# Optimization experiments

Measured on AMD Instinct MI355X. Metric: run time of the kernel, lower is better.

## Reference

```python
import jax, jax.numpy as jnp
import numpy as np

B, T, D = 2, 2048, 1024
H = 16
HD = D // H

def setup_inputs() -> dict:
    key = jax.random.key(0)
    ks = jax.random.split(key, 5)
    s = 1.0 / np.sqrt(D)
    return {
        "x": jax.random.normal(ks[0], (B, T, D), dtype=jnp.float32),
        "Wq": jax.random.normal(ks[1], (D, D), dtype=jnp.float32) * s,
        "bq": jnp.zeros((D,), jnp.float32),
        "Wk": jax.random.normal(ks[2], (D, D), dtype=jnp.float32) * s,
        "bk": jnp.zeros((D,), jnp.float32),
        "Wv": jax.random.normal(ks[3], (D, D), dtype=jnp.float32) * s,
        "bv": jnp.zeros((D,), jnp.float32),
        "Wo": jax.random.normal(ks[4], (D, D), dtype=jnp.float32) * s,
        "bo": jnp.zeros((D,), jnp.float32),
    }

def reference(x, Wq, bq, Wk, bk, Wv, bv, Wo, bo):
    # projections: torch Linear computes x @ W.T + b
    def split_heads(t):  # [B,T,D] -> [B,H,T,HD]
        return t.reshape(B, T, H, HD).transpose(0, 2, 1, 3)
    q = split_heads(x @ Wq.T + bq)
    k = split_heads(x @ Wk.T + bk)
    v = split_heads(x @ Wv.T + bv)
    scale = 1.0 / jnp.sqrt(jnp.asarray(HD, x.dtype))
    scores = jnp.einsum("bhtd,bhsd->bhts", q, k) * scale  # [B,H,T,T]
    causal = jnp.tril(jnp.ones((T, T), bool))
    scores = jnp.where(causal, scores, -jnp.inf)
    attn = jax.nn.softmax(scores, axis=-1)
    out = jnp.einsum("bhts,bhsd->bhtd", attn, v)  # [B,H,T,HD]
    out = out.transpose(0, 2, 1, 3).reshape(B, T, D)
    return out @ Wo.T + bo
```

## Files before the change

### kernel.cpp

```cpp
#include <hip/hip_runtime.h>
#include <hip/hip_bf16.h>

#define B_NUM 2
#define T_LEN 2048
#define D_DIM 1024
#define H_NUM 16
#define HD_DIM 64

#define Q_PRESCALE 0.18033688011112042f

using bf16x8 = __attribute__((ext_vector_type(8))) short;
using f32x4  = __attribute__((ext_vector_type(4))) float;
using u16x4  = __attribute__((ext_vector_type(4))) unsigned short;

__device__ __forceinline__ unsigned short f2bf(float f) {
    union { __hip_bfloat16 b; unsigned short u; } v;
    v.b = __float2bfloat16(f);
    return v.u;
}

__device__ __forceinline__ unsigned pack2bf(float a, float b) {
    union { __hip_bfloat162 h; unsigned u; } v;
    v.h = __float22bfloat162_rn(float2{a, b});
    return v.u;
}

__device__ __forceinline__ void gload16(const unsigned short* g, unsigned short* l) {
    __builtin_amdgcn_global_load_lds(
        (const __attribute__((address_space(1))) void*)g,
        (__attribute__((address_space(3))) void*)l, 16, 0, 0);
}

__global__ __launch_bounds__(256) void cvt5(
    const float* __restrict__ s0, const float* __restrict__ s1, const float* __restrict__ s2,
    const float* __restrict__ s3, const float* __restrict__ s4,
    unsigned short* __restrict__ d0, unsigned short* __restrict__ d1, unsigned short* __restrict__ d2,
    unsigned short* __restrict__ d3, unsigned short* __restrict__ d4,
    int c0, int c1, int c2, int c3, int c4)
{
    const float* src; unsigned short* dst; int cnt;
    switch (blockIdx.z) {
        case 0: src = s0; dst = d0; cnt = c0; break;
        case 1: src = s1; dst = d1; cnt = c1; break;
        case 2: src = s2; dst = d2; cnt = c2; break;
        case 3: src = s3; dst = d3; cnt = c3; break;
        default: src = s4; dst = d4; cnt = c4; break;
    }
    const int stride = gridDim.x * 256 * 4;
    for (int i = (blockIdx.x * 256 + threadIdx.x) * 4; i < cnt; i += stride) {
        float4 v = *(const float4*)(src + i);
        u16x4 o = { f2bf(v.x), f2bf(v.y), f2bf(v.z), f2bf(v.w) };
        *(u16x4*)(dst + i) = o;
    }
}

__device__ __forceinline__ void tile128(
    const unsigned short* __restrict__ A, const unsigned short* __restrict__ Bm,
    int m0, int n0, int K, unsigned short* lds, f32x4 acc[4][4])
{
    const int tid  = threadIdx.x;
    const int lane = tid & 63, w = tid >> 6;
    const int g = lane >> 4, c = lane & 15;
    const int wr = w >> 1, wc = w & 1;
    const int srow = lane >> 2;
    const int sch  = lane & 3;
    const int scsw = sch ^ ((srow >> 1) & 3);
    const int chunk = w * 2;
    const int row0 = chunk * 16 + srow;
    const int row1 = row0 + 16;
    const int rsw = (c >> 1) & 3;

    #pragma unroll
    for (int mi = 0; mi < 4; ++mi)
        #pragma unroll
        for (int ni = 0; ni < 4; ++ni)
            acc[mi][ni] = (f32x4){0.f, 0.f, 0.f, 0.f};

    const unsigned short* gA0 = A  + (size_t)(m0 + row0) * K + scsw * 8;
    const unsigned short* gA1 = A  + (size_t)(m0 + row1) * K + scsw * 8;
    const unsigned short* gB0 = Bm + (size_t)(n0 + row0) * K + scsw * 8;
    const unsigned short* gB1 = Bm + (size_t)(n0 + row1) * K + scsw * 8;

    auto stage = [&](int buf, int k0) {
        unsigned short* bA = lds + buf * 8192;
        unsigned short* bB = bA + 4096;
        gload16(gA0 + k0, bA + chunk * 512);
        gload16(gA1 + k0, bA + (chunk + 1) * 512);
        gload16(gB0 + k0, bB + chunk * 512);
        gload16(gB1 + k0, bB + (chunk + 1) * 512);
    };

    auto kstep = [&](int buf) {
        __builtin_amdgcn_s_barrier();
        asm volatile("" ::: "memory");
        const unsigned short* bA = lds + buf * 8192;
        const unsigned short* bB = bA + 4096;
        bf16x8 af[4], bfr[4];
        #pragma unroll
        for (int mi = 0; mi < 4; ++mi)
            af[mi] = *(const bf16x8*)(bA + (wr * 64 + mi * 16 + c) * 32 + (g ^ rsw) * 8);
        #pragma unroll
        for (int ni = 0; ni < 4; ++ni)
            bfr[ni] = *(const bf16x8*)(bB + (wc * 64 + ni * 16 + c) * 32 + (g ^ rsw) * 8);
        #pragma unroll
        for (int mi = 0; mi < 4; ++mi)
            #pragma unroll
            for (int ni = 0; ni < 4; ++ni)
                acc[mi][ni] = __builtin_amdgcn_mfma_f32_16x16x32_bf16(af[mi], bfr[ni], acc[mi][ni], 0, 0, 0);
        asm volatile("s_waitcnt lgkmcnt(0)" ::: "memory");
        __builtin_amdgcn_s_barrier();
    };

    const int nsteps = K / 32;
    stage(0, 0);
    stage(1, 32);
    int buf = 0;
    #pragma unroll 1
    for (int t = 0; t + 2 < nsteps; ++t) {
        int nb = buf + 2; if (nb >= 3) nb -= 3;
        stage(nb, (t + 2) * 32);
        asm volatile("s_waitcnt vmcnt(8)" ::: "memory");
        kstep(buf);
        ++buf; if (buf == 3) buf = 0;
    }
    asm volatile("s_waitcnt vmcnt(4)" ::: "memory");
    kstep(buf);
    ++buf; if (buf == 3) buf = 0;
    asm volatile("s_waitcnt vmcnt(0)" ::: "memory");
    kstep(buf);
}

__global__ __launch_bounds__(256) void gemm_qkv(
    const unsigned short* __restrict__ X,
    const unsigned short* __restrict__ Wq, const unsigned short* __restrict__ Wk,
    const unsigned short* __restrict__ Wv,
    const float* __restrict__ bq, const float* __restrict__ bk, const float* __restrict__ bv,
    unsigned short* __restrict__ Oq, unsigned short* __restrict__ Ok, unsigned short* __restrict__ OvT)
{
    __shared__ __align__(16) unsigned short lds[3 * 8192];
    const int xcd = blockIdx.x & 7;
    const int s   = blockIdx.x >> 3;
    const int mt  = (xcd >> 1) * 8 + s / 12;
    const int rr  = (xcd & 1) * 12 + s % 12;
    const int z   = rr >> 3;
    const int nt  = rr & 7;

    const int lane = threadIdx.x & 63, w = threadIdx.x >> 6;
    const int g = lane >> 4, c = lane & 15;
    const int wr = w >> 1, wc = w & 1;
    f32x4 acc[4][4];

    if (z < 2) {
        const unsigned short* W = z ? Wk : Wq;
        const float* bias       = z ? bk : bq;
        unsigned short* Ob      = z ? Ok : Oq;
        const float oscale      = z ? 1.0f : Q_PRESCALE;
        const int m0 = mt * 128, n0 = nt * 128;
        tile128(X, W, m0, n0, D_DIM, lds, acc);
        #pragma unroll
        for (int mi = 0; mi < 4; ++mi) {
            #pragma unroll
            for (int ni = 0; ni < 4; ++ni) {
                const int col = n0 + wc * 64 + ni * 16 + c;
                const int h = col >> 6, hd = col & 63;
                const float bb = bias[col];
                #pragma unroll
                for (int r = 0; r < 4; ++r) {
                    const int row = m0 + wr * 64 + mi * 16 + g * 4 + r;
                    const int b_ = row >> 11, t = row & (T_LEN - 1);
                    Ob[((size_t)((b_ * H_NUM + h) * T_LEN + t)) * HD_DIM + hd] =
                        f2bf((acc[mi][ni][r] + bb) * oscale);
                }
            }
        }
    } else {
        const int m0 = nt * 128, n0 = mt * 128;
        tile128(Wv, X, m0, n0, D_DIM, lds, acc);
        #pragma unroll
        for (int mi = 0; mi < 4; ++mi) {
            #pragma unroll
            for (int ni = 0; ni < 4; ++ni) {
                const int j = n0 + wc * 64 + ni * 16 + c;
                const int b_ = j >> 11, t = j & (T_LEN - 1);
                #pragma unroll
                for (int r = 0; r < 4; ++r) {
                    const int f = m0 + wr * 64 + mi * 16 + g * 4 + r;
                    OvT[(size_t)(b_ * D_DIM + f) * T_LEN + t] = f2bf(acc[mi][ni][r] + bv[f]);
                }
            }
        }
    }
}

__global__ __launch_bounds__(256) void gemm_out(
    const unsigned short* __restrict__ A, const unsigned short* __restrict__ W,
    const float* __restrict__ bias, float* __restrict__ Out)
{
    __shared__ __align__(16) unsigned short lds[3 * 8192];
    const int bsw = (blockIdx.x & 7) * 32 + (blockIdx.x >> 3);
    const int mt = bsw >> 3, nt = bsw & 7;
    const int lane = threadIdx.x & 63, w = threadIdx.x >> 6;
    const int g = lane >> 4, c = lane & 15;
    const int m0 = mt * 128, n0 = nt * 128;
    f32x4 acc[4][4];
    tile128(A, W, m0, n0, D_DIM, lds, acc);
    const int wr = w >> 1, wc = w & 1;
    #pragma unroll
    for (int mi = 0; mi < 4; ++mi) {
        #pragma unroll
        for (int ni = 0; ni < 4; ++ni) {
            const int col = n0 + wc * 64 + ni * 16 + c;
            const float bb = bias[col];
            #pragma unroll
            for (int r = 0; r < 4; ++r) {
                const int row = m0 + wr * 64 + mi * 16 + g * 4 + r;
                Out[(size_t)row * D_DIM + col] = acc[mi][ni][r] + bb;
            }
        }
    }
}

__global__ __launch_bounds__(256, 4) void attn(
    const unsigned short* __restrict__ Q, const unsigned short* __restrict__ K,
    const unsigned short* __restrict__ VT, unsigned short* __restrict__ O)
{
    __shared__ __align__(16) unsigned short kv_lds[2][2][64 * 64];
    __shared__ __align__(16) unsigned short plbuf[4][16 * 64];
    const int tid = threadIdx.x, lane = tid & 63, w = tid >> 6;
    const int g = lane >> 4, c = lane & 15;

    const int gid = blockIdx.x;
    const int bh = gid & 31;
    const int jt = (gid < 512) ? (31 - (gid >> 5)) : ((gid - 512) >> 5);
    const int q0b = jt * 64;
    const int qw0 = q0b + w * 16;

    const unsigned short* Qb = Q  + (size_t)bh * T_LEN * HD_DIM;
    const unsigned short* Kb = K  + (size_t)bh * T_LEN * HD_DIM;
    const unsigned short* Vb = VT + (size_t)bh * HD_DIM * T_LEN;
    unsigned short* pl = plbuf[w];

    bf16x8 qf[2];
    #pragma unroll
    for (int kk = 0; kk < 2; ++kk)
        qf[kk] = *(const bf16x8*)(Qb + (size_t)(qw0 + c) * HD_DIM + kk * 32 + g * 8);

    f32x4 acc[4];
    #pragma unroll
    for (int ni = 0; ni < 4; ++ni) acc[ni] = (f32x4){0.f, 0.f, 0.f, 0.f};
    float m2 = -1e30f, l2 = 0.f;

    auto stage = [&](int buf, int kv0) {
        unsigned short* kb = &kv_lds[buf][0][0];
        unsigned short* vb = &kv_lds[buf][1][0];
        #pragma unroll
        for (int rnd = 0; rnd < 2; ++rnd) {
            const int bch = rnd * 256 + w * 64;
            const int row = (bch >> 3) + (lane >> 3);
            const int sc16 = (lane & 7) ^ (row & 7);
            gload16(Kb + (size_t)(kv0 + row) * HD_DIM + sc16 * 8, kb + bch * 8);
            gload16(Vb + (size_t)row * T_LEN + kv0 + sc16 * 8,   vb + bch * 8);
        }
    };

    const int ntiles = jt + 1;
    stage(0, 0);
    if (ntiles > 1) stage(1, 64);
    int cur = 0;
    #pragma unroll 1
    for (int t = 0; t < ntiles; ++t) {
        const int kv0 = t << 6;
        if (t + 1 < ntiles)
            asm volatile("s_waitcnt vmcnt(4)" ::: "memory");
        else
            asm volatile("s_waitcnt vmcnt(0)" ::: "memory");
        __builtin_amdgcn_s_barrier();
        const unsigned short* kb = &kv_lds[cur][0][0];
        const unsigned short* vb = &kv_lds[cur][1][0];

        f32x4 sf[4];
        __builtin_amdgcn_s_setprio(1);
        #pragma unroll
        for (int st = 0; st < 4; ++st) {
            const int rr = st * 16 + c;
            bf16x8 kf0 = *(const bf16x8*)(kb + rr * 64 + ((g       ^ (c & 7)) * 8));
            bf16x8 kf1 = *(const bf16x8*)(kb + rr * 64 + (((4 + g) ^ (c & 7)) * 8));
            f32x4 s = (f32x4){0.f, 0.f, 0.f, 0.f};
            s = __builtin_amdgcn_mfma_f32_16x16x32_bf16(kf0, qf[0], s, 0, 0, 0);
            s = __builtin_amdgcn_mfma_f32_16x16x32_bf16(kf1, qf[1], s, 0, 0, 0);
            sf[st] = s;
        }
        __builtin_amdgcn_s_setprio(0);
        if (t == jt) {
            const int qg = qw0 + c;
            #pragma unroll
            for (int st = 0; st < 4; ++st)
                #pragma unroll
                for (int r = 0; r < 4; ++r) {
                    const int kvg = kv0 + st * 16 + g * 4 + r;
                    sf[st][r] = (kvg <= qg) ? sf[st][r] : -1e30f;
                }
        }
        float ma = fmaxf(fmaxf(sf[0][0], sf[0][1]), sf[0][2]);
        float mb = fmaxf(fmaxf(sf[0][3], sf[1][0]), sf[1][1]);
        float mc = fmaxf(fmaxf(sf[1][2], sf[1][3]), sf[2][0]);
        float md = fmaxf(fmaxf(sf[2][1], sf[2][2]), sf[2][3]);
        float me = fmaxf(fmaxf(sf[3][0], sf[3][1]), sf[3][2]);
        float mx = fmaxf(fmaxf(fmaxf(ma, mb), fmaxf(mc, md)), fmaxf(me, sf[3][3]));
        mx = fmaxf(mx, __shfl_xor(mx, 16));
        mx = fmaxf(mx, __shfl_xor(mx, 32));
        if (__any(mx > m2 + 8.f)) {
            const float mnew = fmaxf(m2, mx);
            const float alpha = __builtin_amdgcn_exp2f(m2 - mnew);
            float ar[4];
            #pragma unroll
            for (int r = 0; r < 4; ++r) ar[r] = __shfl(alpha, g * 4 + r);
            l2 *= alpha;
            #pragma unroll
            for (int ni = 0; ni < 4; ++ni)
                #pragma unroll
                for (int r = 0; r < 4; ++r) acc[ni][r] *= ar[r];
            m2 = mnew;
        }
        float sum = 0.f;
        #pragma unroll
        for (int st = 0; st < 4; ++st)
            #pragma unroll
            for (int r = 0; r < 4; ++r) {
                const float p = __builtin_amdgcn_exp2f(sf[st][r] - m2);
                sf[st][r] = p;
                sum += p;
            }
        sum += __shfl_xor(sum, 16);
        sum += __shfl_xor(sum, 32);
        l2 += sum;
        #pragma unroll
        for (int st = 0; st < 4; ++st) {
            uint2 pk;
            pk.x = pack2bf(sf[st][0], sf[st][1]);
            pk.y = pack2bf(sf[st][2], sf[st][3]);
            const int idx = (c * 64 + st * 16 + g * 4) ^ ((c & 7) << 3);
            *(uint2*)(pl + idx) = pk;
        }
        asm volatile("" ::: "memory");
        bf16x8 pa[2];
        #pragma unroll
        for (int kk = 0; kk < 2; ++kk) {
            const int ridx = (c * 64 + kk * 32 + g * 8) ^ ((c & 7) << 3);
            pa[kk] = *(const bf16x8*)(pl + ridx);
        }
        __builtin_amdgcn_s_setprio(1);
        #pragma unroll
        for (int ni = 0; ni < 4; ++ni) {
            const int rr = ni * 16 + c;
            bf16x8 vf0 = *(const bf16x8*)(vb + rr * 64 + ((g       ^ (c & 7)) * 8));
            bf16x8 vf1 = *(const bf16x8*)(vb + rr * 64 + (((4 + g) ^ (c & 7)) * 8));
            acc[ni] = __builtin_amdgcn_mfma_f32_16x16x32_bf16(pa[0], vf0, acc[ni], 0, 0, 0);
            acc[ni] = __builtin_amdgcn_mfma_f32_16x16x32_bf16(pa[1], vf1, acc[ni], 0, 0, 0);
        }
        __builtin_amdgcn_s_setprio(0);
        asm volatile("s_waitcnt lgkmcnt(0)" ::: "memory");
        __builtin_amdgcn_s_barrier();
        if (t + 2 < ntiles) stage(cur, (t + 2) << 6);
        cur ^= 1;
    }

    const float linv = 1.0f / l2;
    float lr[4];
    #pragma unroll
    for (int r = 0; r < 4; ++r) lr[r] = __shfl(linv, g * 4 + r);
    const int b_ = bh >> 4, h = bh & 15;
    #pragma unroll
    for (int ni = 0; ni < 4; ++ni)
        #pragma unroll
        for (int r = 0; r < 4; ++r) {
            const int q = qw0 + g * 4 + r;
            O[(size_t)(b_ * T_LEN + q) * D_DIM + h * HD_DIM + ni * 16 + c] =
                f2bf(acc[ni][r] * lr[r]);
        }
}

extern "C" void kernel_launch(void* const* d_in, const int* in_sizes, int n_in,
                              void* d_out, int out_size, void* d_ws, size_t ws_size,
                              hipStream_t stream)
{
    const float* x  = (const float*)d_in[0];
    const float* Wq = (const float*)d_in[1];
    const float* bq = (const float*)d_in[2];
    const float* Wk = (const float*)d_in[3];
    const float* bk = (const float*)d_in[4];
    const float* Wv = (const float*)d_in[5];
    const float* bv = (const float*)d_in[6];
    const float* Wo = (const float*)d_in[7];
    const float* bo = (const float*)d_in[8];
    float* out = (float*)d_out;

    char* ws = (char*)d_ws;
    const size_t MB = 1u << 20;
    unsigned short* xb  = (unsigned short*)(ws + 0 * MB);
    unsigned short* wqb = (unsigned short*)(ws + 8 * MB);
    unsigned short* wkb = (unsigned short*)(ws + 10 * MB);
    unsigned short* wvb = (unsigned short*)(ws + 12 * MB);
    unsigned short* wob = (unsigned short*)(ws + 14 * MB);
    unsigned short* qw  = (unsigned short*)(ws + 16 * MB);
    unsigned short* kw  = (unsigned short*)(ws + 24 * MB);
    unsigned short* vtw = (unsigned short*)(ws + 32 * MB);
    unsigned short* ow  = (unsigned short*)(ws + 40 * MB);

    cvt5<<<dim3(1024, 1, 5), dim3(256), 0, stream>>>(
        x, Wq, Wk, Wv, Wo, xb, wqb, wkb, wvb, wob,
        B_NUM * T_LEN * D_DIM, D_DIM * D_DIM, D_DIM * D_DIM, D_DIM * D_DIM, D_DIM * D_DIM);

    gemm_qkv<<<dim3(768), dim3(256), 0, stream>>>(
        xb, wqb, wkb, wvb, bq, bk, bv, qw, kw, vtw);

    attn<<<dim3(1024), dim3(256), 0, stream>>>(qw, kw, vtw, ow);

    gemm_out<<<dim3(256), dim3(256), 0, stream>>>(
        ow, wob, bo, out);
}
```

Baseline: 103.6 us.

## Widen attention KV tile to 128 keys and drop MFMA priority hints

The causal flash-attention kernel now processes 128 keys per iteration instead of 64, doubling the K/V LDS tiles, the per-wave P buffer and the score registers. This halves the number of loop iterations, and with them the barriers and softmax reduction overheads. The mask applies whenever the tile extends past the wave's query rows, so diagonal tiles do partly wasted work. The s_setprio hints are removed, and launch bounds drop to 2 blocks per CU to fit the larger LDS and register footprint, which may reduce latency hiding.

```diff
diff --git a/kernel.cpp b/kernel.cpp
--- a/kernel.cpp
+++ b/kernel.cpp
@@ -220,12 +220,12 @@
     }
 }
 
-__global__ __launch_bounds__(256, 4) void attn(
+__global__ __launch_bounds__(256, 2) void attn(
     const unsigned short* __restrict__ Q, const unsigned short* __restrict__ K,
     const unsigned short* __restrict__ VT, unsigned short* __restrict__ O)
 {
-    __shared__ __align__(16) unsigned short kv_lds[2][2][64 * 64];
-    __shared__ __align__(16) unsigned short plbuf[4][16 * 64];
+    __shared__ __align__(16) unsigned short kv_lds[2][2][8192];
+    __shared__ __align__(16) unsigned short plbuf[4][16 * 128];
     const int tid = threadIdx.x, lane = tid & 63, w = tid >> 6;
     const int g = lane >> 4, c = lane & 15;
 
@@ -254,34 +254,35 @@
         unsigned short* kb = &kv_lds[buf][0][0];
         unsigned short* vb = &kv_lds[buf][1][0];
         #pragma unroll
-        for (int rnd = 0; rnd < 2; ++rnd) {
+        for (int rnd = 0; rnd < 4; ++rnd) {
             const int bch = rnd * 256 + w * 64;
-            const int row = (bch >> 3) + (lane >> 3);
-            const int sc16 = (lane & 7) ^ (row & 7);
-            gload16(Kb + (size_t)(kv0 + row) * HD_DIM + sc16 * 8, kb + bch * 8);
-            gload16(Vb + (size_t)row * T_LEN + kv0 + sc16 * 8,   vb + bch * 8);
+            const int krow = (bch >> 3) + (lane >> 3);
+            const int ku = (lane & 7) ^ (krow & 7);
+            gload16(Kb + (size_t)(kv0 + krow) * HD_DIM + ku * 8, kb + bch * 8);
+            const int vrow = (bch >> 4) + (lane >> 4);
+            const int vu = (lane & 15) ^ (vrow & 7);
+            gload16(Vb + (size_t)vrow * T_LEN + kv0 + vu * 8, vb + bch * 8);
         }
     };
 
-    const int ntiles = jt + 1;
+    const int ntiles = (q0b + 191) >> 7;
     stage(0, 0);
-    if (ntiles > 1) stage(1, 64);
+    if (ntiles > 1) stage(1, 128);
     int cur = 0;
     #pragma unroll 1
     for (int t = 0; t < ntiles; ++t) {
-        const int kv0 = t << 6;
+        const int kv0 = t << 7;
         if (t + 1 < ntiles)
-            asm volatile("s_waitcnt vmcnt(4)" ::: "memory");
+            asm volatile("s_waitcnt vmcnt(8)" ::: "memory");
         else
             asm volatile("s_waitcnt vmcnt(0)" ::: "memory");
         __builtin_amdgcn_s_barrier();
         const unsigned short* kb = &kv_lds[cur][0][0];
         const unsigned short* vb = &kv_lds[cur][1][0];
 
-        f32x4 sf[4];
-        __builtin_amdgcn_s_setprio(1);
-        #pragma unroll
-        for (int st = 0; st < 4; ++st) {
+        f32x4 sf[8];
+        #pragma unroll
+        for (int st = 0; st < 8; ++st) {
             const int rr = st * 16 + c;
             bf16x8 kf0 = *(const bf16x8*)(kb + rr * 64 + ((g       ^ (c & 7)) * 8));
             bf16x8 kf1 = *(const bf16x8*)(kb + rr * 64 + (((4 + g) ^ (c & 7)) * 8));
@@ -290,23 +291,22 @@
             s = __builtin_amdgcn_mfma_f32_16x16x32_bf16(kf1, qf[1], s, 0, 0, 0);
             sf[st] = s;
         }
-        __builtin_amdgcn_s_setprio(0);
-        if (t == jt) {
+        if (kv0 + 127 > qw0) {
             const int qg = qw0 + c;
             #pragma unroll
-            for (int st = 0; st < 4; ++st)
+            for (int st = 0; st < 8; ++st)
                 #pragma unroll
                 for (int r = 0; r < 4; ++r) {
                     const int kvg = kv0 + st * 16 + g * 4 + r;
                     sf[st][r] = (kvg <= qg) ? sf[st][r] : -1e30f;
                 }
         }
-        float ma = fmaxf(fmaxf(sf[0][0], sf[0][1]), sf[0][2]);
-        float mb = fmaxf(fmaxf(sf[0][3], sf[1][0]), sf[1][1]);
-        float mc = fmaxf(fmaxf(sf[1][2], sf[1][3]), sf[2][0]);
-        float md = fmaxf(fmaxf(sf[2][1], sf[2][2]), sf[2][3]);
-        float me = fmaxf(fmaxf(sf[3][0], sf[3][1]), sf[3][2]);
-        float mx = fmaxf(fmaxf(fmaxf(ma, mb), fmaxf(mc, md)), fmaxf(me, sf[3][3]));
+        float pm[8];
+        #pragma unroll
+        for (int st = 0; st < 8; ++st)
+            pm[st] = fmaxf(fmaxf(sf[st][0], sf[st][1]), fmaxf(sf[st][2], sf[st][3]));
+        float mx = fmaxf(fmaxf(fmaxf(pm[0], pm[1]), fmaxf(pm[2], pm[3])),
+                         fmaxf(fmaxf(pm[4], pm[5]), fmaxf(pm[6], pm[7])));
         mx = fmaxf(mx, __shfl_xor(mx, 16));
         mx = fmaxf(mx, __shfl_xor(mx, 32));
         if (__any(mx > m2 + 8.f)) {
@@ -324,7 +324,7 @@
         }
         float sum = 0.f;
         #pragma unroll
-        for (int st = 0; st < 4; ++st)
+        for (int st = 0; st < 8; ++st)
             #pragma unroll
             for (int r = 0; r < 4; ++r) {
                 const float p = __builtin_amdgcn_exp2f(sf[st][r] - m2);
@@ -335,33 +335,32 @@
         sum += __shfl_xor(sum, 32);
         l2 += sum;
         #pragma unroll
-        for (int st = 0; st < 4; ++st) {
+        for (int st = 0; st < 8; ++st) {
             uint2 pk;
             pk.x = pack2bf(sf[st][0], sf[st][1]);
             pk.y = pack2bf(sf[st][2], sf[st][3]);
-            const int idx = (c * 64 + st * 16 + g * 4) ^ ((c & 7) << 3);
+            const int idx = (c * 128 + st * 16 + g * 4) ^ ((c & 7) << 3);
             *(uint2*)(pl + idx) = pk;
         }
         asm volatile("" ::: "memory");
-        bf16x8 pa[2];
-        #pragma unroll
-        for (int kk = 0; kk < 2; ++kk) {
-            const int ridx = (c * 64 + kk * 32 + g * 8) ^ ((c & 7) << 3);
+        bf16x8 pa[4];
+        #pragma unroll
+        for (int kk = 0; kk < 4; ++kk) {
+            const int ridx = (c * 128 + kk * 32 + g * 8) ^ ((c & 7) << 3);
             pa[kk] = *(const bf16x8*)(pl + ridx);
         }
-        __builtin_amdgcn_s_setprio(1);
         #pragma unroll
         for (int ni = 0; ni < 4; ++ni) {
-            const int rr = ni * 16 + c;
-            bf16x8 vf0 = *(const bf16x8*)(vb + rr * 64 + ((g       ^ (c & 7)) * 8));
-            bf16x8 vf1 = *(const bf16x8*)(vb + rr * 64 + (((4 + g) ^ (c & 7)) * 8));
-            acc[ni] = __builtin_amdgcn_mfma_f32_16x16x32_bf16(pa[0], vf0, acc[ni], 0, 0, 0);
-            acc[ni] = __builtin_amdgcn_mfma_f32_16x16x32_bf16(pa[1], vf1, acc[ni], 0, 0, 0);
-        }
-        __builtin_amdgcn_s_setprio(0);
+            const int vrow = (ni * 16 + c) * 128;
+            #pragma unroll
+            for (int kk = 0; kk < 4; ++kk) {
+                bf16x8 vf = *(const bf16x8*)(vb + vrow + (((kk * 4 + g) ^ (c & 7)) * 8));
+                acc[ni] = __builtin_amdgcn_mfma_f32_16x16x32_bf16(pa[kk], vf, acc[ni], 0, 0, 0);
+            }
+        }
         asm volatile("s_waitcnt lgkmcnt(0)" ::: "memory");
         __builtin_amdgcn_s_barrier();
-        if (t + 2 < ntiles) stage(cur, (t + 2) << 6);
+        if (t + 2 < ntiles) stage(cur, (t + 2) << 7);
         cur ^= 1;
     }
 
```

New measurement: 114.0 us. 1.1x slower.
